# Kernel optimization log

Measured on AMD Instinct MI355X. Metric: run time of the kernel, lower is better.

## Reference

```python
import jax, jax.numpy as jnp
import numpy as np

NEG = -1e30  # log-zero surrogate (avoid -inf for stable grads)


def ctc_neg_log_like(log_probs, targets, input_lengths, target_lengths):
    """Standard CTC (blank=0) negative log-likelihood, mean over batch.
    Math-equivalent to k2 topo-compile + intersect_dense + log-semiring tot_scores.
    log_probs: [B,T,C] logits or log-probs (re-normalized, as GradExpNormalize does).
    """
    lp = jax.nn.log_softmax(log_probs, axis=-1)
    B, T, C = lp.shape
    S = targets.shape[1]
    L = 2 * S + 1  # blank-interleaved extended label sequence length
    ext = jnp.zeros((B, L), jnp.int32).at[:, 1::2].set(targets.astype(jnp.int32))
    prev2 = jnp.pad(ext[:, :-2], ((0, 0), (2, 0)), constant_values=-1)
    can_skip = (ext != prev2) & (ext != 0)  # skip transition allowed

    lp_tb = jnp.moveaxis(lp, 1, 0)  # [T,B,C] for scan over time
    start = jnp.full((B, L), NEG, lp.dtype).at[:, 0].set(0.0).at[:, 1].set(0.0)
    alpha0 = start + jnp.take_along_axis(lp_tb[0], ext, axis=1)  # [B,L]

    def step(alpha, xs):
        lp_t, t = xs
        emit_t = jnp.take_along_axis(lp_t, ext, axis=1)  # [B,L]
        s1 = jnp.pad(alpha[:, :-1], ((0, 0), (1, 0)), constant_values=NEG)
        s2 = jnp.where(can_skip,
                       jnp.pad(alpha[:, :-2], ((0, 0), (2, 0)), constant_values=NEG),
                       NEG)
        new = jnp.logaddexp(jnp.logaddexp(alpha, s1), s2) + emit_t
        # freeze alpha once past this utterance's length
        new = jnp.where((t < input_lengths)[:, None], new, alpha)
        return new, None

    ts = jnp.arange(1, T, dtype=jnp.int32)
    alpha, _ = jax.lax.scan(step, alpha0, (lp_tb[1:], ts))

    idx1 = (2 * target_lengths).astype(jnp.int32)
    idx2 = jnp.maximum(2 * target_lengths - 1, 0).astype(jnp.int32)
    a1 = jnp.take_along_axis(alpha, idx1[:, None], axis=1)[:, 0]
    a2 = jnp.take_along_axis(alpha, idx2[:, None], axis=1)[:, 0]
    a2 = jnp.where(target_lengths > 0, a2, NEG)
    tot_scores = jnp.logaddexp(a1, a2)  # per-utterance log-likelihood
    return -jnp.mean(tot_scores)  # reduction='mean'


def setup_inputs() -> dict:
    key = jax.random.key(0)
    k1, k2, k3, k4 = jax.random.split(key, 4)
    B, T, C, S = 64, 2048, 1024, 256
    log_probs = jax.random.normal(k1, (B, T, C), dtype=jnp.float32)
    targets = 1 + jax.random.randint(k2, (B, S), 0, C - 1, dtype=jnp.int32)  # labels in [1, C)
    input_lengths = jax.random.randint(k3, (B,), T // 2, T + 1, dtype=jnp.int32)
    target_lengths = jax.random.randint(k4, (B,), S // 2, S + 1, dtype=jnp.int32)
    return {"log_probs": log_probs, "targets": targets,
            "input_lengths": input_lengths, "target_lengths": target_lengths}


def reference(log_probs, targets, input_lengths, target_lengths):
    return ctc_neg_log_like(log_probs, targets, input_lengths, target_lengths)
```

## Files before the change

kernel.cpp:

```cpp
#include <hip/hip_runtime.h>
#include <math.h>

typedef __attribute__((ext_vector_type(4))) float f32x4;

#define SB() __builtin_amdgcn_sched_barrier(0)
#define WAITV(n)                                              \
  do {                                                        \
    asm volatile("s_waitcnt vmcnt(" #n ")" ::: "memory");     \
    SB();                                                     \
  } while (0)
#define LD4(dst, ptr, OFF)                                           \
  asm volatile("global_load_dwordx4 %0, %1, off offset:" OFF         \
               : "=v"(dst) : "v"(ptr) : "memory")
#define LD1(dst, ptr, OFF)                                           \
  asm volatile("global_load_dword %0, %1, off offset:" OFF           \
               : "=v"(dst) : "v"(ptr) : "memory")

__device__ inline float wave_max64(float v) {
#pragma unroll
  for (int off = 32; off > 0; off >>= 1) v = fmaxf(v, __shfl_xor(v, off, 64));
  return v;
}
__device__ inline float wave_sum64(float v) {
#pragma unroll
  for (int off = 32; off > 0; off >>= 1) v += __shfl_xor(v, off, 64);
  return v;
}
__device__ inline float wave_max_dpp(float x) {
  int xi = __float_as_int(x);
  x = fmaxf(x, __int_as_float(__builtin_amdgcn_update_dpp(xi, xi, 0x111, 0xf, 0xf, false)));
  xi = __float_as_int(x);
  x = fmaxf(x, __int_as_float(__builtin_amdgcn_update_dpp(xi, xi, 0x112, 0xf, 0xf, false)));
  xi = __float_as_int(x);
  x = fmaxf(x, __int_as_float(__builtin_amdgcn_update_dpp(xi, xi, 0x114, 0xf, 0xf, false)));
  xi = __float_as_int(x);
  x = fmaxf(x, __int_as_float(__builtin_amdgcn_update_dpp(xi, xi, 0x118, 0xf, 0xf, false)));
  xi = __float_as_int(x);
  x = fmaxf(x, __int_as_float(__builtin_amdgcn_update_dpp(xi, xi, 0x142, 0xa, 0xf, false)));
  xi = __float_as_int(x);
  x = fmaxf(x, __int_as_float(__builtin_amdgcn_update_dpp(xi, xi, 0x143, 0xc, 0xf, false)));
  return __int_as_float(__builtin_amdgcn_readlane(__float_as_int(x), 63));
}
__device__ inline float lane_shr1(float x) {
  return __int_as_float(__builtin_amdgcn_update_dpp(
      0, __float_as_int(x), 0x138, 0xf, 0xf, true));
}

__device__ __forceinline__ void k1_body(
    const float* __restrict__ lp, const int* __restrict__ targets,
    float* __restrict__ gw, int t0, int T, int Tc, int CB, int S,
    int b, int tq, float* rowbuf) {
  const int lane = threadIdx.x & 63;
  const int w = threadIdx.x >> 6;
  const int tloc = tq * 4 + w;
  const int t = t0 + tloc;
  if (t >= T) return;
  const int4 tg4 = *(const int4*)(targets + (size_t)b * S + 4 * lane);

  const float* row = lp + ((size_t)b * T + t) * 1024;
  const float4 v0 = *(const float4*)(row + 4 * lane);
  const float4 v1 = *(const float4*)(row + 256 + 4 * lane);
  const float4 v2 = *(const float4*)(row + 512 + 4 * lane);
  const float4 v3 = *(const float4*)(row + 768 + 4 * lane);
  float mx = fmaxf(fmaxf(fmaxf(v0.x, v0.y), fmaxf(v0.z, v0.w)),
                   fmaxf(fmaxf(v1.x, v1.y), fmaxf(v1.z, v1.w)));
  mx = fmaxf(mx, fmaxf(fmaxf(fmaxf(v2.x, v2.y), fmaxf(v2.z, v2.w)),
                       fmaxf(fmaxf(v3.x, v3.y), fmaxf(v3.z, v3.w))));
  mx = wave_max64(mx);
  float sm = __expf(v0.x - mx) + __expf(v0.y - mx) + __expf(v0.z - mx) +
             __expf(v0.w - mx) + __expf(v1.x - mx) + __expf(v1.y - mx) +
             __expf(v1.z - mx) + __expf(v1.w - mx) + __expf(v2.x - mx) +
             __expf(v2.y - mx) + __expf(v2.z - mx) + __expf(v2.w - mx) +
             __expf(v3.x - mx) + __expf(v3.y - mx) + __expf(v3.z - mx) +
             __expf(v3.w - mx);
  sm = wave_sum64(sm);
  const float lse = mx + __logf(sm);
  *(float4*)(rowbuf + 4 * lane) = v0;
  *(float4*)(rowbuf + 256 + 4 * lane) = v1;
  *(float4*)(rowbuf + 512 + 4 * lane) = v2;
  *(float4*)(rowbuf + 768 + 4 * lane) = v3;
  const float e0 = __expf(rowbuf[tg4.x] - lse);
  const float e1 = __expf(rowbuf[tg4.y] - lse);
  const float e2 = __expf(rowbuf[tg4.z] - lse);
  const float e3 = __expf(rowbuf[tg4.w] - lse);
  float* gr = gw + ((size_t)b * CB + tloc) * 272;
  *(float4*)(gr + 4 * lane) = make_float4(e0, e1, e2, e3);
  if (lane == 0) gr[256] = __expf(rowbuf[0] - lse);
}

__global__ __launch_bounds__(256) void k1_std(
    const float* __restrict__ lp, const int* __restrict__ targets,
    float* __restrict__ gw, int t0, int T, int Tc, int CB, int S) {
  __shared__ __align__(16) float rowbuf4[4][1024];
  k1_body(lp, targets, gw, t0, T, Tc, CB, S, blockIdx.y, blockIdx.x,
          rowbuf4[threadIdx.x >> 6]);
}

#define DECL8(P)                                                     \
  f32x4 P##v0, P##v1, P##v2, P##v3, P##v4, P##v5, P##v6, P##v7;      \
  float P##q0, P##q1, P##q2, P##q3, P##q4, P##q5, P##q6, P##q7;

#define ISS8(P)                                                      \
  do {                                                               \
    LD4(P##v0, gpA_, "0");    LD1(P##q0, gqA_, "0");                 \
    LD4(P##v1, gpA_, "1088"); LD1(P##q1, gqA_, "1088");              \
    LD4(P##v2, gpA_, "2176"); LD1(P##q2, gqA_, "2176");              \
    LD4(P##v3, gpA_, "3264"); LD1(P##q3, gqA_, "3264");              \
    LD4(P##v4, gpB_, "0");    LD1(P##q4, gqB_, "0");                 \
    LD4(P##v5, gpB_, "1088"); LD1(P##q5, gqB_, "1088");              \
    LD4(P##v6, gpB_, "2176"); LD1(P##q6, gqB_, "2176");              \
    LD4(P##v7, gpB_, "3264"); LD1(P##q7, gqB_, "3264");              \
    gpA_ += 2176; gqA_ += 2176; gpB_ += 2176; gqB_ += 2176;          \
  } while (0)

#define KSR(pv, qv)                                              \
  {                                                              \
    const float hm1 = lane_shr1(a7);                             \
    const float n0 = (a0 + hm1) * (qv);                          \
    const float n1 = __fmaf_rn(sk1, hm1, a1 + a0) * (pv).x;      \
    const float n2 = (a2 + a1) * (qv);                           \
    const float n3 = __fmaf_rn(sk3, a1, a3 + a2) * (pv).y;       \
    const float n4 = (a4 + a3) * (qv);                           \
    const float n5 = __fmaf_rn(sk5, a3, a5 + a4) * (pv).z;       \
    const float n6 = (a6 + a5) * (qv);                           \
    const float n7 = __fmaf_rn(sk7, a5, a7 + a6) * (pv).w;       \
    const float n8 = (a8 + a7) * (qv);                           \
    a0 = n0; a1 = n1; a2 = n2; a3 = n3; a4 = n4;                 \
    a5 = n5; a6 = n6; a7 = n7; a8 = n8;                          \
  }

#define RESC()                                                            \
  {                                                                       \
    float m_ = fmaxf(fmaxf(fmaxf(fmaxf(a0, a1), fmaxf(a2, a3)),           \
                           fmaxf(fmaxf(a4, a5), fmaxf(a6, a7))), a8);     \
    m_ = wave_max_dpp(m_);                                                \
    const int e_ =                                                        \
        (m_ > 0.f) ? (int)((__float_as_uint(m_) >> 23) & 255u) - 127 : 0; \
    a0 = ldexpf(a0, -e_); a1 = ldexpf(a1, -e_); a2 = ldexpf(a2, -e_);     \
    a3 = ldexpf(a3, -e_); a4 = ldexpf(a4, -e_); a5 = ldexpf(a5, -e_);     \
    a6 = ldexpf(a6, -e_); a7 = ldexpf(a7, -e_); a8 = ldexpf(a8, -e_);     \
    E += e_;                                                              \
  }

#define COMP8(P, rem)                                            \
  do {                                                           \
    if ((rem) >= 8) {                                            \
      KSR(P##v0, P##q0) KSR(P##v1, P##q1) KSR(P##v2, P##q2)      \
      KSR(P##v3, P##q3) KSR(P##v4, P##q4) KSR(P##v5, P##q5)      \
      KSR(P##v6, P##q6) KSR(P##v7, P##q7) RESC()                 \
    } else {                                                     \
      KSR(P##v0, P##q0)                                          \
      if ((rem) > 1) KSR(P##v1, P##q1)                           \
      if ((rem) > 2) KSR(P##v2, P##q2)                           \
      if ((rem) > 3) KSR(P##v3, P##q3)                           \
      if ((rem) > 4) KSR(P##v4, P##q4)                           \
      if ((rem) > 5) KSR(P##v5, P##q5)                           \
      if ((rem) > 6) KSR(P##v6, P##q6)                           \
      RESC()                                                     \
    }                                                            \
  } while (0)

template <int R0, int LAST>
__device__ __forceinline__ void k2_body(
    const float* __restrict__ gb, const int* __restrict__ targets,
    const int* __restrict__ in_len, const int* __restrict__ tgt_len,
    float* __restrict__ alpha_g, int* __restrict__ exp_g,
    float* __restrict__ tot, int b, int t0, int Tc, int S) {
  const int lane = threadIdx.x & 63;
  const int len = in_len[b];
  const int tl = tgt_len[b];
  const int* tg = targets + (size_t)b * S;
  const int4 mytg = *(const int4*)(tg + 4 * lane);
  const int tgm1 = (lane > 0) ? tg[4 * lane - 1] : -1;
  const float sk1 = (lane > 0 && mytg.x != tgm1) ? 1.f : 0.f;
  const float sk3 = (mytg.y != mytg.x) ? 1.f : 0.f;
  const float sk5 = (mytg.z != mytg.y) ? 1.f : 0.f;
  const float sk7 = (mytg.w != mytg.z) ? 1.f : 0.f;

  float a0 = 0.f, a1 = 0.f, a2 = 0.f, a3 = 0.f, a4 = 0.f, a5 = 0.f, a6 = 0.f,
        a7 = 0.f, a8 = 0.f;
  int E = 0;
  if (R0) {
    if (lane == 0) { a0 = gb[256]; a1 = gb[0]; }
  } else {
    const float* ap = alpha_g + (size_t)b * 520 + 8 * lane;
    a0 = ap[0]; a1 = ap[1]; a2 = ap[2]; a3 = ap[3];
    a4 = ap[4]; a5 = ap[5]; a6 = ap[6]; a7 = ap[7];
    a8 = (lane == 63) ? alpha_g[(size_t)b * 520 + 512] : 0.f;
    E = exp_g[b];
  }

  const int t_hi = min(t0 + Tc, len);
  int N = t_hi - (t0 + R0);
  if (N < 0) N = 0;
  const int G = (N + 7) >> 3;

  const float* gpA_ = gb + (size_t)R0 * 272 + 4 * lane;
  const float* gqA_ = gb + (size_t)R0 * 272 + 256;
  const float* gpB_ = gpA_ + 1088;
  const float* gqB_ = gqA_ + 1088;

  DECL8(A) DECL8(B)

  __builtin_amdgcn_s_setprio(1);
  asm volatile("s_waitcnt vmcnt(0) lgkmcnt(0)" ::: "memory");
  SB();
  ISS8(A); ISS8(B);

  for (int g = 0; g < G; g += 2) {
    WAITV(16);
    COMP8(A, N - 8 * g);
    ISS8(A);
    if (g + 1 < G) {
      WAITV(16);
      COMP8(B, N - 8 * (g + 1));
      ISS8(B);
    }
  }
  WAITV(0);
  __builtin_amdgcn_s_setprio(0);

  if constexpr (LAST) {
    __shared__ float fin[520];
    fin[8 * lane + 0] = a0; fin[8 * lane + 1] = a1;
    fin[8 * lane + 2] = a2; fin[8 * lane + 3] = a3;
    fin[8 * lane + 4] = a4; fin[8 * lane + 5] = a5;
    fin[8 * lane + 6] = a6; fin[8 * lane + 7] = a7;
    if (lane == 63) fin[512] = a8;
    asm volatile("s_waitcnt lgkmcnt(0)" ::: "memory");
    SB();
    if (lane == 0) {
      const int i1 = 2 * tl;
      const int i2 = (2 * tl - 1 > 0) ? (2 * tl - 1) : 0;
      float v = fin[i1] + ((tl > 0) ? fin[i2] : 0.f);
      v = fmaxf(v, 1e-37f);
      tot[b] = logf(v) + (float)E * 0.6931471805599453f;
    }
  } else {
    float* ap = alpha_g + (size_t)b * 520 + 8 * lane;
    ap[0] = a0; ap[1] = a1; ap[2] = a2; ap[3] = a3;
    ap[4] = a4; ap[5] = a5; ap[6] = a6; ap[7] = a7;
    if (lane == 63) alpha_g[(size_t)b * 520 + 512] = a8;
    if (lane == 0) exp_g[b] = E;
  }
}

template <int R0, int LAST>
__global__ __launch_bounds__(64, 1) void k2_std(
    const float* __restrict__ gbuf, const int* __restrict__ targets,
    const int* __restrict__ in_len, const int* __restrict__ tgt_len,
    float* __restrict__ alpha_g, int* __restrict__ exp_g,
    float* __restrict__ tot, int t0, int Tc, int CB, int S) {
  k2_body<R0, LAST>(gbuf + (size_t)blockIdx.x * CB * 272, targets, in_len,
                    tgt_len, alpha_g, exp_g, tot, blockIdx.x, t0, Tc, S);
}

template <int R0>
__global__ __launch_bounds__(256, 1) void fused_k(
    const float* __restrict__ lp, const int* __restrict__ targets,
    const int* __restrict__ in_len, const int* __restrict__ tgt_len,
    float* __restrict__ alpha_g, int* __restrict__ exp_g,
    float* __restrict__ tot, const float* __restrict__ gprev,
    float* __restrict__ gcur, int t0k2, int t0k1, int T, int Tc, int CB,
    int S, int TQ4) {
  __shared__ __align__(16) float rowbuf4[4][1024];
  if (blockIdx.x < 64) {
    if (threadIdx.x >= 64) return;
    k2_body<R0, 0>(gprev + (size_t)blockIdx.x * CB * 272, targets, in_len,
                   tgt_len, alpha_g, exp_g, tot, blockIdx.x, t0k2, Tc, S);
    return;
  }
  const int id = blockIdx.x - 64;
  const int b = id / TQ4;
  const int tq = id - b * TQ4;
  k1_body(lp, targets, gcur, t0k1, T, Tc, CB, S, b, tq,
          rowbuf4[threadIdx.x >> 6]);
}

__global__ void k3_mean(const float* __restrict__ tot, float* __restrict__ out,
                        int B) {
  float v = (threadIdx.x < B) ? tot[threadIdx.x] : 0.0f;
  v = wave_sum64(v);
  if (threadIdx.x == 0) out[0] = -v / (float)B;
}

extern "C" void kernel_launch(void* const* d_in, const int* in_sizes, int n_in,
                              void* d_out, int out_size, void* d_ws,
                              size_t ws_size, hipStream_t stream) {
  const float* lp = (const float*)d_in[0];
  const int* targets = (const int*)d_in[1];
  const int* in_len = (const int*)d_in[2];
  const int* tgt_len = (const int*)d_in[3];
  float* out = (float*)d_out;

  const int B = in_sizes[2];
  const int S = in_sizes[1] / B;
  const int C = 1024;
  const int T = (int)((size_t)in_sizes[0] / ((size_t)B * C));

  const size_t headf = 64 + 64 + (size_t)64 * 520;
  int Tc = 512;
  if (Tc > T) Tc = T;
  while (Tc > 64) {
    const size_t need =
        headf * 4 + 2 * (size_t)64 * (Tc + 64) * 272 * 4;
    if (need <= ws_size) break;
    Tc >>= 1;
  }
  const int CB = Tc + 64;
  const int nch = (T + Tc - 1) / Tc;
  const int TQ4 = Tc / 4;

  float* tot = (float*)d_ws;
  int* exp_g = (int*)(tot + 64);
  float* alpha_g = (float*)(exp_g + 64);
  float* g0 = alpha_g + (size_t)64 * 520;
  const size_t BUF = (size_t)64 * CB * 272;
  float* gbuf[2] = {g0, g0 + BUF};

  if (nch == 1) {
    k1_std<<<dim3(TQ4, B), 256, 0, stream>>>(lp, targets, gbuf[0], 0, T, Tc,
                                             CB, S);
    k2_std<1, 1><<<B, 64, 0, stream>>>(gbuf[0], targets, in_len, tgt_len,
                                       alpha_g, exp_g, tot, 0, Tc, CB, S);
  } else {
    k1_std<<<dim3(TQ4, B), 256, 0, stream>>>(lp, targets, gbuf[0], 0, T, Tc,
                                             CB, S);
    for (int c = 1; c < nch; ++c) {
      const int t0k2 = (c - 1) * Tc;
      const int t0k1 = c * Tc;
      const dim3 grid(64 + TQ4 * B);
      if (c == 1)
        fused_k<1><<<grid, 256, 0, stream>>>(
            lp, targets, in_len, tgt_len, alpha_g, exp_g, tot,
            gbuf[(c - 1) & 1], gbuf[c & 1], t0k2, t0k1, T, Tc, CB, S, TQ4);
      else
        fused_k<0><<<grid, 256, 0, stream>>>(
            lp, targets, in_len, tgt_len, alpha_g, exp_g, tot,
            gbuf[(c - 1) & 1], gbuf[c & 1], t0k2, t0k1, T, Tc, CB, S, TQ4);
    }
    const int cl = nch - 1;
    k2_std<0, 1><<<B, 64, 0, stream>>>(gbuf[cl & 1], targets, in_len, tgt_len,
                                       alpha_g, exp_g, tot, cl * Tc, Tc, CB,
                                       S);
  }
  k3_mean<<<1, 64, 0, stream>>>(tot, out, B);
}
```

Measured before the change: 233.5 us.

## Pack eight waves per block and triple-buffer the alpha recursion loads

Blocks now hold 8 waves (512 threads) instead of 4. The recursion stage (k2) packs 8 batch rows per block, so it runs on 8 blocks instead of 64 single-wave blocks. The k2 inner loop moves from double to triple buffering of the 8-step load groups (vmcnt 32), which keeps more loads in flight to hide global latency on the serial alpha chain. The risks are higher register pressure from the third buffer set, and 8 recursion waves now sharing one CU instead of spreading across 64 CUs, which could slow the latency-bound sequential part.

```diff
diff --git a/kernel.cpp b/kernel.cpp
--- a/kernel.cpp
+++ b/kernel.cpp
@@ -46,13 +46,13 @@
       0, __float_as_int(x), 0x138, 0xf, 0xf, true));
 }
 
-__device__ __forceinline__ void k1_body(
+__device__ __forceinline__ void k1_body8(
     const float* __restrict__ lp, const int* __restrict__ targets,
-    float* __restrict__ gw, int t0, int T, int Tc, int CB, int S,
+    float* __restrict__ gw, int t0, int T, int CB, int S,
     int b, int tq, float* rowbuf) {
   const int lane = threadIdx.x & 63;
   const int w = threadIdx.x >> 6;
-  const int tloc = tq * 4 + w;
+  const int tloc = tq * 8 + w;
   const int t = t0 + tloc;
   if (t >= T) return;
   const int4 tg4 = *(const int4*)(targets + (size_t)b * S + 4 * lane);
@@ -88,12 +88,12 @@
   if (lane == 0) gr[256] = __expf(rowbuf[0] - lse);
 }
 
-__global__ __launch_bounds__(256) void k1_std(
+__global__ __launch_bounds__(512, 2) void k1_std8(
     const float* __restrict__ lp, const int* __restrict__ targets,
-    float* __restrict__ gw, int t0, int T, int Tc, int CB, int S) {
-  __shared__ __align__(16) float rowbuf4[4][1024];
-  k1_body(lp, targets, gw, t0, T, Tc, CB, S, blockIdx.y, blockIdx.x,
-          rowbuf4[threadIdx.x >> 6]);
+    float* __restrict__ gw, int t0, int T, int CB, int S) {
+  __shared__ __align__(16) float lds[8192];
+  k1_body8(lp, targets, gw, t0, T, CB, S, blockIdx.y, blockIdx.x,
+           lds + (threadIdx.x >> 6) * 1024);
 }
 
 #define DECL8(P)                                                     \
@@ -165,7 +165,7 @@
     const float* __restrict__ gb, const int* __restrict__ targets,
     const int* __restrict__ in_len, const int* __restrict__ tgt_len,
     float* __restrict__ alpha_g, int* __restrict__ exp_g,
-    float* __restrict__ tot, int b, int t0, int Tc, int S) {
+    float* __restrict__ tot, int b, int t0, int Tc, int S, float* fin) {
   const int lane = threadIdx.x & 63;
   const int len = in_len[b];
   const int tl = tgt_len[b];
@@ -200,28 +200,32 @@
   const float* gpB_ = gpA_ + 1088;
   const float* gqB_ = gqA_ + 1088;
 
-  DECL8(A) DECL8(B)
+  DECL8(A) DECL8(B) DECL8(C)
 
   __builtin_amdgcn_s_setprio(1);
   asm volatile("s_waitcnt vmcnt(0) lgkmcnt(0)" ::: "memory");
   SB();
-  ISS8(A); ISS8(B);
-
-  for (int g = 0; g < G; g += 2) {
-    WAITV(16);
+  ISS8(A); ISS8(B); ISS8(C);
+
+  for (int g = 0; g < G; g += 3) {
+    WAITV(32);
     COMP8(A, N - 8 * g);
     ISS8(A);
     if (g + 1 < G) {
-      WAITV(16);
+      WAITV(32);
       COMP8(B, N - 8 * (g + 1));
       ISS8(B);
     }
+    if (g + 2 < G) {
+      WAITV(32);
+      COMP8(C, N - 8 * (g + 2));
+      ISS8(C);
+    }
   }
   WAITV(0);
   __builtin_amdgcn_s_setprio(0);
 
   if constexpr (LAST) {
-    __shared__ float fin[520];
     fin[8 * lane + 0] = a0; fin[8 * lane + 1] = a1;
     fin[8 * lane + 2] = a2; fin[8 * lane + 3] = a3;
     fin[8 * lane + 4] = a4; fin[8 * lane + 5] = a5;
@@ -246,35 +250,38 @@
 }
 
 template <int R0, int LAST>
-__global__ __launch_bounds__(64, 1) void k2_std(
+__global__ __launch_bounds__(512, 2) void k2_std8(
     const float* __restrict__ gbuf, const int* __restrict__ targets,
     const int* __restrict__ in_len, const int* __restrict__ tgt_len,
     float* __restrict__ alpha_g, int* __restrict__ exp_g,
     float* __restrict__ tot, int t0, int Tc, int CB, int S) {
-  k2_body<R0, LAST>(gbuf + (size_t)blockIdx.x * CB * 272, targets, in_len,
-                    tgt_len, alpha_g, exp_g, tot, blockIdx.x, t0, Tc, S);
+  __shared__ float fin[4160];
+  const int w = threadIdx.x >> 6;
+  const int b = blockIdx.x * 8 + w;
+  k2_body<R0, LAST>(gbuf + (size_t)b * CB * 272, targets, in_len, tgt_len,
+                    alpha_g, exp_g, tot, b, t0, Tc, S, fin + w * 520);
 }
 
 template <int R0>
-__global__ __launch_bounds__(256, 1) void fused_k(
+__global__ __launch_bounds__(512, 2) void fused8(
     const float* __restrict__ lp, const int* __restrict__ targets,
     const int* __restrict__ in_len, const int* __restrict__ tgt_len,
     float* __restrict__ alpha_g, int* __restrict__ exp_g,
     float* __restrict__ tot, const float* __restrict__ gprev,
     float* __restrict__ gcur, int t0k2, int t0k1, int T, int Tc, int CB,
-    int S, int TQ4) {
-  __shared__ __align__(16) float rowbuf4[4][1024];
-  if (blockIdx.x < 64) {
-    if (threadIdx.x >= 64) return;
-    k2_body<R0, 0>(gprev + (size_t)blockIdx.x * CB * 272, targets, in_len,
-                   tgt_len, alpha_g, exp_g, tot, blockIdx.x, t0k2, Tc, S);
+    int S, int TQ8) {
+  __shared__ __align__(16) float lds[8192];
+  const int w = threadIdx.x >> 6;
+  if (blockIdx.x < 8) {
+    const int b = blockIdx.x * 8 + w;
+    k2_body<R0, 0>(gprev + (size_t)b * CB * 272, targets, in_len, tgt_len,
+                   alpha_g, exp_g, tot, b, t0k2, Tc, S, lds + w * 520);
     return;
   }
-  const int id = blockIdx.x - 64;
-  const int b = id / TQ4;
-  const int tq = id - b * TQ4;
-  k1_body(lp, targets, gcur, t0k1, T, Tc, CB, S, b, tq,
-          rowbuf4[threadIdx.x >> 6]);
+  const int id = blockIdx.x - 8;
+  const int b = id / TQ8;
+  const int tq = id - b * TQ8;
+  k1_body8(lp, targets, gcur, t0k1, T, CB, S, b, tq, lds + w * 1024);
 }
 
 __global__ void k3_mean(const float* __restrict__ tot, float* __restrict__ out,
@@ -302,14 +309,13 @@
   int Tc = 512;
   if (Tc > T) Tc = T;
   while (Tc > 64) {
-    const size_t need =
-        headf * 4 + 2 * (size_t)64 * (Tc + 64) * 272 * 4;
+    const size_t need = headf * 4 + 2 * (size_t)64 * (Tc + 64) * 272 * 4;
     if (need <= ws_size) break;
     Tc >>= 1;
   }
   const int CB = Tc + 64;
   const int nch = (T + Tc - 1) / Tc;
-  const int TQ4 = Tc / 4;
+  const int TQ8 = Tc / 8;
 
   float* tot = (float*)d_ws;
   int* exp_g = (int*)(tot + 64);
@@ -319,30 +325,30 @@
   float* gbuf[2] = {g0, g0 + BUF};
 
   if (nch == 1) {
-    k1_std<<<dim3(TQ4, B), 256, 0, stream>>>(lp, targets, gbuf[0], 0, T, Tc,
-                                             CB, S);
-    k2_std<1, 1><<<B, 64, 0, stream>>>(gbuf[0], targets, in_len, tgt_len,
-                                       alpha_g, exp_g, tot, 0, Tc, CB, S);
+    k1_std8<<<dim3(TQ8, B), 512, 0, stream>>>(lp, targets, gbuf[0], 0, T, CB,
+                                              S);
+    k2_std8<1, 1><<<8, 512, 0, stream>>>(gbuf[0], targets, in_len, tgt_len,
+                                         alpha_g, exp_g, tot, 0, Tc, CB, S);
   } else {
-    k1_std<<<dim3(TQ4, B), 256, 0, stream>>>(lp, targets, gbuf[0], 0, T, Tc,
-                                             CB, S);
+    k1_std8<<<dim3(TQ8, B), 512, 0, stream>>>(lp, targets, gbuf[0], 0, T, CB,
+                                              S);
     for (int c = 1; c < nch; ++c) {
       const int t0k2 = (c - 1) * Tc;
       const int t0k1 = c * Tc;
-      const dim3 grid(64 + TQ4 * B);
+      const dim3 grid(8 + TQ8 * B);
       if (c == 1)
-        fused_k<1><<<grid, 256, 0, stream>>>(
+        fused8<1><<<grid, 512, 0, stream>>>(
             lp, targets, in_len, tgt_len, alpha_g, exp_g, tot,
-            gbuf[(c - 1) & 1], gbuf[c & 1], t0k2, t0k1, T, Tc, CB, S, TQ4);
+            gbuf[(c - 1) & 1], gbuf[c & 1], t0k2, t0k1, T, Tc, CB, S, TQ8);
       else
-        fused_k<0><<<grid, 256, 0, stream>>>(
+        fused8<0><<<grid, 512, 0, stream>>>(
             lp, targets, in_len, tgt_len, alpha_g, exp_g, tot,
-            gbuf[(c - 1) & 1], gbuf[c & 1], t0k2, t0k1, T, Tc, CB, S, TQ4);
+            gbuf[(c - 1) & 1], gbuf[c & 1], t0k2, t0k1, T, Tc, CB, S, TQ8);
     }
     const int cl = nch - 1;
-    k2_std<0, 1><<<B, 64, 0, stream>>>(gbuf[cl & 1], targets, in_len, tgt_len,
-                                       alpha_g, exp_g, tot, cl * Tc, Tc, CB,
-                                       S);
+    k2_std8<0, 1><<<8, 512, 0, stream>>>(gbuf[cl & 1], targets, in_len,
+                                         tgt_len, alpha_g, exp_g, tot,
+                                         cl * Tc, Tc, CB, S);
   }
   k3_mean<<<1, 64, 0, stream>>>(tot, out, B);
 }
```

New measurement: 324.4 us. 38.9% more time.

## Pair two utterances per recursion wave and split blank emissions into separate array

Applied to the files above, without the earlier changes.

The serial CTC forward recursion now runs two batch items interleaved in one wave, so 32 recursion waves replace 64 and each wave has two independent dependency chains to hide latency. The blank emission probabilities move out of the padded 272-float rows into a contiguous per-batch array, which allows vector loads for blanks and 256-float label rows. The cost is twice the register state per wave, a deeper load pipeline, and a loop length set by the longer of the two utterances.

```diff
diff --git a/kernel.cpp b/kernel.cpp
--- a/kernel.cpp
+++ b/kernel.cpp
@@ -11,9 +11,6 @@
   } while (0)
 #define LD4(dst, ptr, OFF)                                           \
   asm volatile("global_load_dwordx4 %0, %1, off offset:" OFF         \
-               : "=v"(dst) : "v"(ptr) : "memory")
-#define LD1(dst, ptr, OFF)                                           \
-  asm volatile("global_load_dword %0, %1, off offset:" OFF           \
                : "=v"(dst) : "v"(ptr) : "memory")
 
 __device__ inline float wave_max64(float v) {
@@ -48,8 +45,8 @@
 
 __device__ __forceinline__ void k1_body(
     const float* __restrict__ lp, const int* __restrict__ targets,
-    float* __restrict__ gw, int t0, int T, int Tc, int CB, int S,
-    int b, int tq, float* rowbuf) {
+    float* __restrict__ gw, float* __restrict__ qw, int t0, int T, int CB,
+    int QS, int S, int b, int tq, float* rowbuf) {
   const int lane = threadIdx.x & 63;
   const int w = threadIdx.x >> 6;
   const int tloc = tq * 4 + w;
@@ -83,198 +80,256 @@
   const float e1 = __expf(rowbuf[tg4.y] - lse);
   const float e2 = __expf(rowbuf[tg4.z] - lse);
   const float e3 = __expf(rowbuf[tg4.w] - lse);
-  float* gr = gw + ((size_t)b * CB + tloc) * 272;
+  float* gr = gw + ((size_t)b * CB + tloc) * 256;
   *(float4*)(gr + 4 * lane) = make_float4(e0, e1, e2, e3);
-  if (lane == 0) gr[256] = __expf(rowbuf[0] - lse);
+  if (lane == 0) qw[(size_t)b * QS + tloc] = __expf(rowbuf[0] - lse);
 }
 
 __global__ __launch_bounds__(256) void k1_std(
     const float* __restrict__ lp, const int* __restrict__ targets,
-    float* __restrict__ gw, int t0, int T, int Tc, int CB, int S) {
+    float* __restrict__ gw, float* __restrict__ qw, int t0, int T, int CB,
+    int QS, int S) {
   __shared__ __align__(16) float rowbuf4[4][1024];
-  k1_body(lp, targets, gw, t0, T, Tc, CB, S, blockIdx.y, blockIdx.x,
+  k1_body(lp, targets, gw, qw, t0, T, CB, QS, S, blockIdx.y, blockIdx.x,
           rowbuf4[threadIdx.x >> 6]);
 }
 
-#define DECL8(P)                                                     \
-  f32x4 P##v0, P##v1, P##v2, P##v3, P##v4, P##v5, P##v6, P##v7;      \
-  float P##q0, P##q1, P##q2, P##q3, P##q4, P##q5, P##q6, P##q7;
-
-#define ISS8(P)                                                      \
+#define DECLSET(P) \
+  f32x4 P##v0, P##v1, P##v2, P##v3, P##v4, P##v5, P##v6, P##v7, P##qL, P##qH;
+
+#define ISS8(P, B)                                                   \
   do {                                                               \
-    LD4(P##v0, gpA_, "0");    LD1(P##q0, gqA_, "0");                 \
-    LD4(P##v1, gpA_, "1088"); LD1(P##q1, gqA_, "1088");              \
-    LD4(P##v2, gpA_, "2176"); LD1(P##q2, gqA_, "2176");              \
-    LD4(P##v3, gpA_, "3264"); LD1(P##q3, gqA_, "3264");              \
-    LD4(P##v4, gpB_, "0");    LD1(P##q4, gqB_, "0");                 \
-    LD4(P##v5, gpB_, "1088"); LD1(P##q5, gqB_, "1088");              \
-    LD4(P##v6, gpB_, "2176"); LD1(P##q6, gqB_, "2176");              \
-    LD4(P##v7, gpB_, "3264"); LD1(P##q7, gqB_, "3264");              \
-    gpA_ += 2176; gqA_ += 2176; gpB_ += 2176; gqB_ += 2176;          \
+    LD4(P##v0, B##gp0, "0");    LD4(P##v1, B##gp0, "1024");          \
+    LD4(P##v2, B##gp0, "2048"); LD4(P##v3, B##gp0, "3072");          \
+    LD4(P##v4, B##gp1, "0");    LD4(P##v5, B##gp1, "1024");          \
+    LD4(P##v6, B##gp1, "2048"); LD4(P##v7, B##gp1, "3072");          \
+    LD4(P##qL, B##gq, "0");     LD4(P##qH, B##gq, "16");             \
+    B##gp0 += 2048; B##gp1 += 2048; B##gq += 8;                      \
   } while (0)
 
-#define KSR(pv, qv)                                              \
-  {                                                              \
-    const float hm1 = lane_shr1(a7);                             \
-    const float n0 = (a0 + hm1) * (qv);                          \
-    const float n1 = __fmaf_rn(sk1, hm1, a1 + a0) * (pv).x;      \
-    const float n2 = (a2 + a1) * (qv);                           \
-    const float n3 = __fmaf_rn(sk3, a1, a3 + a2) * (pv).y;       \
-    const float n4 = (a4 + a3) * (qv);                           \
-    const float n5 = __fmaf_rn(sk5, a3, a5 + a4) * (pv).z;       \
-    const float n6 = (a6 + a5) * (qv);                           \
-    const float n7 = __fmaf_rn(sk7, a5, a7 + a6) * (pv).w;       \
-    const float n8 = (a8 + a7) * (qv);                           \
-    a0 = n0; a1 = n1; a2 = n2; a3 = n3; a4 = n4;                 \
-    a5 = n5; a6 = n6; a7 = n7; a8 = n8;                          \
-  }
-
-#define RESC()                                                            \
-  {                                                                       \
-    float m_ = fmaxf(fmaxf(fmaxf(fmaxf(a0, a1), fmaxf(a2, a3)),           \
-                           fmaxf(fmaxf(a4, a5), fmaxf(a6, a7))), a8);     \
-    m_ = wave_max_dpp(m_);                                                \
-    const int e_ =                                                        \
-        (m_ > 0.f) ? (int)((__float_as_uint(m_) >> 23) & 255u) - 127 : 0; \
-    a0 = ldexpf(a0, -e_); a1 = ldexpf(a1, -e_); a2 = ldexpf(a2, -e_);     \
-    a3 = ldexpf(a3, -e_); a4 = ldexpf(a4, -e_); a5 = ldexpf(a5, -e_);     \
-    a6 = ldexpf(a6, -e_); a7 = ldexpf(a7, -e_); a8 = ldexpf(a8, -e_);     \
-    E += e_;                                                              \
-  }
-
-#define COMP8(P, rem)                                            \
-  do {                                                           \
-    if ((rem) >= 8) {                                            \
-      KSR(P##v0, P##q0) KSR(P##v1, P##q1) KSR(P##v2, P##q2)      \
-      KSR(P##v3, P##q3) KSR(P##v4, P##q4) KSR(P##v5, P##q5)      \
-      KSR(P##v6, P##q6) KSR(P##v7, P##q7) RESC()                 \
-    } else {                                                     \
-      KSR(P##v0, P##q0)                                          \
-      if ((rem) > 1) KSR(P##v1, P##q1)                           \
-      if ((rem) > 2) KSR(P##v2, P##q2)                           \
-      if ((rem) > 3) KSR(P##v3, P##q3)                           \
-      if ((rem) > 4) KSR(P##v4, P##q4)                           \
-      if ((rem) > 5) KSR(P##v5, P##q5)                           \
-      if ((rem) > 6) KSR(P##v6, P##q6)                           \
-      RESC()                                                     \
-    }                                                            \
+#define KSR(B, pv, qv)                                                 \
+  {                                                                    \
+    const float hm1 = lane_shr1(B##a7);                                \
+    const float n0 = (B##a0 + hm1) * (qv);                             \
+    const float n1 = __fmaf_rn(B##sk1, hm1, B##a1 + B##a0) * (pv).x;   \
+    const float n2 = (B##a2 + B##a1) * (qv);                           \
+    const float n3 = __fmaf_rn(B##sk3, B##a1, B##a3 + B##a2) * (pv).y; \
+    const float n4 = (B##a4 + B##a3) * (qv);                           \
+    const float n5 = __fmaf_rn(B##sk5, B##a3, B##a5 + B##a4) * (pv).z; \
+    const float n6 = (B##a6 + B##a5) * (qv);                           \
+    const float n7 = __fmaf_rn(B##sk7, B##a5, B##a7 + B##a6) * (pv).w; \
+    const float n8 = (B##a8 + B##a7) * (qv);                           \
+    B##a0 = n0; B##a1 = n1; B##a2 = n2; B##a3 = n3; B##a4 = n4;        \
+    B##a5 = n5; B##a6 = n6; B##a7 = n7; B##a8 = n8;                    \
+  }
+
+#define RESC(B)                                                              \
+  {                                                                          \
+    float m_ = fmaxf(fmaxf(fmaxf(fmaxf(B##a0, B##a1), fmaxf(B##a2, B##a3)),  \
+                           fmaxf(fmaxf(B##a4, B##a5), fmaxf(B##a6, B##a7))), \
+                     B##a8);                                                 \
+    m_ = wave_max_dpp(m_);                                                   \
+    const int e_ =                                                           \
+        (m_ > 0.f) ? (int)((__float_as_uint(m_) >> 23) & 255u) - 127 : 0;    \
+    B##a0 = ldexpf(B##a0, -e_); B##a1 = ldexpf(B##a1, -e_);                  \
+    B##a2 = ldexpf(B##a2, -e_); B##a3 = ldexpf(B##a3, -e_);                  \
+    B##a4 = ldexpf(B##a4, -e_); B##a5 = ldexpf(B##a5, -e_);                  \
+    B##a6 = ldexpf(B##a6, -e_); B##a7 = ldexpf(B##a7, -e_);                  \
+    B##a8 = ldexpf(B##a8, -e_);                                              \
+    B##E += e_;                                                              \
+  }
+
+#define COMP8(P, B, rem)                                             \
+  do {                                                               \
+    if ((rem) > 0) {                                                 \
+      if ((rem) >= 8) {                                              \
+        KSR(B, P##v0, (P##qL).x) KSR(B, P##v1, (P##qL).y)            \
+        KSR(B, P##v2, (P##qL).z) KSR(B, P##v3, (P##qL).w)            \
+        KSR(B, P##v4, (P##qH).x) KSR(B, P##v5, (P##qH).y)            \
+        KSR(B, P##v6, (P##qH).z) KSR(B, P##v7, (P##qH).w)            \
+        RESC(B)                                                      \
+      } else {                                                       \
+        KSR(B, P##v0, (P##qL).x)                                     \
+        if ((rem) > 1) KSR(B, P##v1, (P##qL).y)                      \
+        if ((rem) > 2) KSR(B, P##v2, (P##qL).z)                      \
+        if ((rem) > 3) KSR(B, P##v3, (P##qL).w)                      \
+        if ((rem) > 4) KSR(B, P##v4, (P##qH).x)                      \
+        if ((rem) > 5) KSR(B, P##v5, (P##qH).y)                      \
+        if ((rem) > 6) KSR(B, P##v6, (P##qH).z)                      \
+        RESC(B)                                                      \
+      }                                                              \
+    }                                                                \
   } while (0)
 
+#define SAVEB(B, bidx)                                                      \
+  {                                                                         \
+    float* ap = alpha_g + (size_t)(bidx)*520 + 8 * lane;                    \
+    ap[0] = B##a0; ap[1] = B##a1; ap[2] = B##a2; ap[3] = B##a3;             \
+    ap[4] = B##a4; ap[5] = B##a5; ap[6] = B##a6; ap[7] = B##a7;             \
+    if (lane == 63) alpha_g[(size_t)(bidx)*520 + 512] = B##a8;              \
+    if (lane == 0) exp_g[bidx] = B##E;                                      \
+  }
+
 template <int R0, int LAST>
-__device__ __forceinline__ void k2_body(
-    const float* __restrict__ gb, const int* __restrict__ targets,
-    const int* __restrict__ in_len, const int* __restrict__ tgt_len,
-    float* __restrict__ alpha_g, int* __restrict__ exp_g,
-    float* __restrict__ tot, int b, int t0, int Tc, int S) {
+__device__ __forceinline__ void k2_pair_body(
+    const float* __restrict__ gwc, const float* __restrict__ qwc,
+    const int* __restrict__ targets, const int* __restrict__ in_len,
+    const int* __restrict__ tgt_len, float* __restrict__ alpha_g,
+    int* __restrict__ exp_g, float* __restrict__ tot, int bA, int t0, int Tc,
+    int CB, int QS, int S, float* finA, float* finB) {
   const int lane = threadIdx.x & 63;
-  const int len = in_len[b];
-  const int tl = tgt_len[b];
-  const int* tg = targets + (size_t)b * S;
-  const int4 mytg = *(const int4*)(tg + 4 * lane);
-  const int tgm1 = (lane > 0) ? tg[4 * lane - 1] : -1;
-  const float sk1 = (lane > 0 && mytg.x != tgm1) ? 1.f : 0.f;
-  const float sk3 = (mytg.y != mytg.x) ? 1.f : 0.f;
-  const float sk5 = (mytg.z != mytg.y) ? 1.f : 0.f;
-  const float sk7 = (mytg.w != mytg.z) ? 1.f : 0.f;
-
-  float a0 = 0.f, a1 = 0.f, a2 = 0.f, a3 = 0.f, a4 = 0.f, a5 = 0.f, a6 = 0.f,
-        a7 = 0.f, a8 = 0.f;
-  int E = 0;
+  const int bB = bA + 1;
+  const float* gA_ = gwc + (size_t)bA * CB * 256;
+  const float* gB_ = gwc + (size_t)bB * CB * 256;
+  const float* qA_ = qwc + (size_t)bA * QS;
+  const float* qB_ = qwc + (size_t)bB * QS;
+
+  float Ask1, Ask3, Ask5, Ask7, Bsk1, Bsk3, Bsk5, Bsk7;
+  {
+    const int* tg_ = targets + (size_t)bA * S;
+    const int4 t4_ = *(const int4*)(tg_ + 4 * lane);
+    const int tm1_ = (lane > 0) ? tg_[4 * lane - 1] : -1;
+    Ask1 = (lane > 0 && t4_.x != tm1_) ? 1.f : 0.f;
+    Ask3 = (t4_.y != t4_.x) ? 1.f : 0.f;
+    Ask5 = (t4_.z != t4_.y) ? 1.f : 0.f;
+    Ask7 = (t4_.w != t4_.z) ? 1.f : 0.f;
+  }
+  {
+    const int* tg_ = targets + (size_t)bB * S;
+    const int4 t4_ = *(const int4*)(tg_ + 4 * lane);
+    const int tm1_ = (lane > 0) ? tg_[4 * lane - 1] : -1;
+    Bsk1 = (lane > 0 && t4_.x != tm1_) ? 1.f : 0.f;
+    Bsk3 = (t4_.y != t4_.x) ? 1.f : 0.f;
+    Bsk5 = (t4_.z != t4_.y) ? 1.f : 0.f;
+    Bsk7 = (t4_.w != t4_.z) ? 1.f : 0.f;
+  }
+
+  float Aa0 = 0.f, Aa1 = 0.f, Aa2 = 0.f, Aa3 = 0.f, Aa4 = 0.f, Aa5 = 0.f,
+        Aa6 = 0.f, Aa7 = 0.f, Aa8 = 0.f;
+  float Ba0 = 0.f, Ba1 = 0.f, Ba2 = 0.f, Ba3 = 0.f, Ba4 = 0.f, Ba5 = 0.f,
+        Ba6 = 0.f, Ba7 = 0.f, Ba8 = 0.f;
+  int AE = 0, BE = 0;
   if (R0) {
-    if (lane == 0) { a0 = gb[256]; a1 = gb[0]; }
+    if (lane == 0) {
+      Aa0 = qA_[0]; Aa1 = gA_[0];
+      Ba0 = qB_[0]; Ba1 = gB_[0];
+    }
   } else {
-    const float* ap = alpha_g + (size_t)b * 520 + 8 * lane;
-    a0 = ap[0]; a1 = ap[1]; a2 = ap[2]; a3 = ap[3];
-    a4 = ap[4]; a5 = ap[5]; a6 = ap[6]; a7 = ap[7];
-    a8 = (lane == 63) ? alpha_g[(size_t)b * 520 + 512] : 0.f;
-    E = exp_g[b];
-  }
-
-  const int t_hi = min(t0 + Tc, len);
-  int N = t_hi - (t0 + R0);
-  if (N < 0) N = 0;
-  const int G = (N + 7) >> 3;
-
-  const float* gpA_ = gb + (size_t)R0 * 272 + 4 * lane;
-  const float* gqA_ = gb + (size_t)R0 * 272 + 256;
-  const float* gpB_ = gpA_ + 1088;
-  const float* gqB_ = gqA_ + 1088;
-
-  DECL8(A) DECL8(B)
+    const float* ap = alpha_g + (size_t)bA * 520 + 8 * lane;
+    Aa0 = ap[0]; Aa1 = ap[1]; Aa2 = ap[2]; Aa3 = ap[3];
+    Aa4 = ap[4]; Aa5 = ap[5]; Aa6 = ap[6]; Aa7 = ap[7];
+    const float* bp = alpha_g + (size_t)bB * 520 + 8 * lane;
+    Ba0 = bp[0]; Ba1 = bp[1]; Ba2 = bp[2]; Ba3 = bp[3];
+    Ba4 = bp[4]; Ba5 = bp[5]; Ba6 = bp[6]; Ba7 = bp[7];
+    if (lane == 63) {
+      Aa8 = alpha_g[(size_t)bA * 520 + 512];
+      Ba8 = alpha_g[(size_t)bB * 520 + 512];
+    }
+    AE = exp_g[bA]; BE = exp_g[bB];
+  }
+
+  const int lenA = in_len[bA], lenB = in_len[bB];
+  const int tlA = tgt_len[bA], tlB = tgt_len[bB];
+  int NA = min(t0 + Tc, lenA) - (t0 + R0); if (NA < 0) NA = 0;
+  int NB = min(t0 + Tc, lenB) - (t0 + R0); if (NB < 0) NB = 0;
+  const int G = ((NA > NB ? NA : NB) + 7) >> 3;
+
+  const float* Agp0 = gA_ + (size_t)R0 * 256 + 4 * lane;
+  const float* Agp1 = Agp0 + 1024;
+  const float* Agq = qA_ + R0;
+  const float* Bgp0 = gB_ + (size_t)R0 * 256 + 4 * lane;
+  const float* Bgp1 = Bgp0 + 1024;
+  const float* Bgq = qB_ + R0;
+
+  DECLSET(XA) DECLSET(XB) DECLSET(YA) DECLSET(YB)
 
   __builtin_amdgcn_s_setprio(1);
   asm volatile("s_waitcnt vmcnt(0) lgkmcnt(0)" ::: "memory");
   SB();
-  ISS8(A); ISS8(B);
+  ISS8(XA, A); ISS8(XB, B); ISS8(YA, A); ISS8(YB, B);
 
   for (int g = 0; g < G; g += 2) {
-    WAITV(16);
-    COMP8(A, N - 8 * g);
-    ISS8(A);
-    if (g + 1 < G) {
-      WAITV(16);
-      COMP8(B, N - 8 * (g + 1));
-      ISS8(B);
-    }
+    WAITV(20);
+    COMP8(XA, A, NA - 8 * g);
+    COMP8(XB, B, NB - 8 * g);
+    ISS8(XA, A); ISS8(XB, B);
+    WAITV(20);
+    COMP8(YA, A, NA - 8 * (g + 1));
+    COMP8(YB, B, NB - 8 * (g + 1));
+    ISS8(YA, A); ISS8(YB, B);
   }
   WAITV(0);
   __builtin_amdgcn_s_setprio(0);
 
   if constexpr (LAST) {
-    __shared__ float fin[520];
-    fin[8 * lane + 0] = a0; fin[8 * lane + 1] = a1;
-    fin[8 * lane + 2] = a2; fin[8 * lane + 3] = a3;
-    fin[8 * lane + 4] = a4; fin[8 * lane + 5] = a5;
-    fin[8 * lane + 6] = a6; fin[8 * lane + 7] = a7;
-    if (lane == 63) fin[512] = a8;
+    finA[8 * lane + 0] = Aa0; finA[8 * lane + 1] = Aa1;
+    finA[8 * lane + 2] = Aa2; finA[8 * lane + 3] = Aa3;
+    finA[8 * lane + 4] = Aa4; finA[8 * lane + 5] = Aa5;
+    finA[8 * lane + 6] = Aa6; finA[8 * lane + 7] = Aa7;
+    finB[8 * lane + 0] = Ba0; finB[8 * lane + 1] = Ba1;
+    finB[8 * lane + 2] = Ba2; finB[8 * lane + 3] = Ba3;
+    finB[8 * lane + 4] = Ba4; finB[8 * lane + 5] = Ba5;
+    finB[8 * lane + 6] = Ba6; finB[8 * lane + 7] = Ba7;
+    if (lane == 63) { finA[512] = Aa8; finB[512] = Ba8; }
     asm volatile("s_waitcnt lgkmcnt(0)" ::: "memory");
     SB();
     if (lane == 0) {
-      const int i1 = 2 * tl;
-      const int i2 = (2 * tl - 1 > 0) ? (2 * tl - 1) : 0;
-      float v = fin[i1] + ((tl > 0) ? fin[i2] : 0.f);
-      v = fmaxf(v, 1e-37f);
-      tot[b] = logf(v) + (float)E * 0.6931471805599453f;
+      {
+        const int i1 = 2 * tlA;
+        const int i2 = (2 * tlA - 1 > 0) ? (2 * tlA - 1) : 0;
+        float v = finA[i1] + ((tlA > 0) ? finA[i2] : 0.f);
+        v = fmaxf(v, 1e-37f);
+        tot[bA] = logf(v) + (float)AE * 0.6931471805599453f;
+      }
+      {
+        const int i1 = 2 * tlB;
+        const int i2 = (2 * tlB - 1 > 0) ? (2 * tlB - 1) : 0;
+        float v = finB[i1] + ((tlB > 0) ? finB[i2] : 0.f);
+        v = fmaxf(v, 1e-37f);
+        tot[bB] = logf(v) + (float)BE * 0.6931471805599453f;
+      }
     }
   } else {
-    float* ap = alpha_g + (size_t)b * 520 + 8 * lane;
-    ap[0] = a0; ap[1] = a1; ap[2] = a2; ap[3] = a3;
-    ap[4] = a4; ap[5] = a5; ap[6] = a6; ap[7] = a7;
-    if (lane == 63) alpha_g[(size_t)b * 520 + 512] = a8;
-    if (lane == 0) exp_g[b] = E;
+    SAVEB(A, bA)
+    SAVEB(B, bB)
   }
 }
 
 template <int R0, int LAST>
-__global__ __launch_bounds__(64, 1) void k2_std(
-    const float* __restrict__ gbuf, const int* __restrict__ targets,
-    const int* __restrict__ in_len, const int* __restrict__ tgt_len,
-    float* __restrict__ alpha_g, int* __restrict__ exp_g,
-    float* __restrict__ tot, int t0, int Tc, int CB, int S) {
-  k2_body<R0, LAST>(gbuf + (size_t)blockIdx.x * CB * 272, targets, in_len,
-                    tgt_len, alpha_g, exp_g, tot, blockIdx.x, t0, Tc, S);
+__global__ __launch_bounds__(64, 1) void k2p_std(
+    const float* __restrict__ gwc, const float* __restrict__ qwc,
+    const int* __restrict__ targets, const int* __restrict__ in_len,
+    const int* __restrict__ tgt_len, float* __restrict__ alpha_g,
+    int* __restrict__ exp_g, float* __restrict__ tot, int t0, int Tc, int CB,
+    int QS, int S) {
+  __shared__ float fin[1040];
+  k2_pair_body<R0, LAST>(gwc, qwc, targets, in_len, tgt_len, alpha_g, exp_g,
+                         tot, blockIdx.x * 2, t0, Tc, CB, QS, S, fin,
+                         fin + 520);
 }
 
 template <int R0>
-__global__ __launch_bounds__(256, 1) void fused_k(
+__global__ __launch_bounds__(256, 1) void fusedp(
     const float* __restrict__ lp, const int* __restrict__ targets,
     const int* __restrict__ in_len, const int* __restrict__ tgt_len,
     float* __restrict__ alpha_g, int* __restrict__ exp_g,
     float* __restrict__ tot, const float* __restrict__ gprev,
-    float* __restrict__ gcur, int t0k2, int t0k1, int T, int Tc, int CB,
-    int S, int TQ4) {
-  __shared__ __align__(16) float rowbuf4[4][1024];
-  if (blockIdx.x < 64) {
+    const float* __restrict__ qprev, float* __restrict__ gcur,
+    float* __restrict__ qcur, int t0k2, int t0k1, int T, int Tc, int CB,
+    int QS, int S, int TQ4) {
+  __shared__ __align__(16) float lds[4096];
+  if (blockIdx.x < 32) {
     if (threadIdx.x >= 64) return;
-    k2_body<R0, 0>(gprev + (size_t)blockIdx.x * CB * 272, targets, in_len,
-                   tgt_len, alpha_g, exp_g, tot, blockIdx.x, t0k2, Tc, S);
+    k2_pair_body<R0, 0>(gprev, qprev, targets, in_len, tgt_len, alpha_g,
+                        exp_g, tot, blockIdx.x * 2, t0k2, Tc, CB, QS, S,
+                        nullptr, nullptr);
     return;
   }
-  const int id = blockIdx.x - 64;
+  const int id = blockIdx.x - 32;
   const int b = id / TQ4;
   const int tq = id - b * TQ4;
-  k1_body(lp, targets, gcur, t0k1, T, Tc, CB, S, b, tq,
-          rowbuf4[threadIdx.x >> 6]);
+  k1_body(lp, targets, gcur, qcur, t0k1, T, CB, QS, S, b, tq,
+          lds + (threadIdx.x >> 6) * 1024);
 }
 
 __global__ void k3_mean(const float* __restrict__ tot, float* __restrict__ out,
@@ -301,48 +356,56 @@
   const size_t headf = 64 + 64 + (size_t)64 * 520;
   int Tc = 512;
   if (Tc > T) Tc = T;
-  while (Tc > 64) {
-    const size_t need =
-        headf * 4 + 2 * (size_t)64 * (Tc + 64) * 272 * 4;
-    if (need <= ws_size) break;
+  int CB = 0, QS = 0;
+  while (Tc >= 64) {
+    CB = Tc + 64;
+    QS = Tc + 64;
+    const size_t need = (headf + 2 * (size_t)64 * QS) * 4 +
+                        2 * (size_t)64 * CB * 1024 + (size_t)80 * 1024;
+    if (need <= ws_size || Tc == 64) break;
     Tc >>= 1;
   }
-  const int CB = Tc + 64;
   const int nch = (T + Tc - 1) / Tc;
   const int TQ4 = Tc / 4;
 
   float* tot = (float*)d_ws;
   int* exp_g = (int*)(tot + 64);
   float* alpha_g = (float*)(exp_g + 64);
-  float* g0 = alpha_g + (size_t)64 * 520;
-  const size_t BUF = (size_t)64 * CB * 272;
-  float* gbuf[2] = {g0, g0 + BUF};
+  float* q0 = alpha_g + (size_t)64 * 520;
+  float* q1 = q0 + (size_t)64 * QS;
+  float* g0 = q1 + (size_t)64 * QS;
+  float* g1 = g0 + (size_t)64 * CB * 256;
+  float* gbuf[2] = {g0, g1};
+  float* qbuf[2] = {q0, q1};
 
   if (nch == 1) {
-    k1_std<<<dim3(TQ4, B), 256, 0, stream>>>(lp, targets, gbuf[0], 0, T, Tc,
-                                             CB, S);
-    k2_std<1, 1><<<B, 64, 0, stream>>>(gbuf[0], targets, in_len, tgt_len,
-                                       alpha_g, exp_g, tot, 0, Tc, CB, S);
+    k1_std<<<dim3(TQ4, B), 256, 0, stream>>>(lp, targets, gbuf[0], qbuf[0], 0,
+                                             T, CB, QS, S);
+    k2p_std<1, 1><<<32, 64, 0, stream>>>(gbuf[0], qbuf[0], targets, in_len,
+                                         tgt_len, alpha_g, exp_g, tot, 0, Tc,
+                                         CB, QS, S);
   } else {
-    k1_std<<<dim3(TQ4, B), 256, 0, stream>>>(lp, targets, gbuf[0], 0, T, Tc,
-                                             CB, S);
+    k1_std<<<dim3(TQ4, B), 256, 0, stream>>>(lp, targets, gbuf[0], qbuf[0], 0,
+                                             T, CB, QS, S);
     for (int c = 1; c < nch; ++c) {
       const int t0k2 = (c - 1) * Tc;
       const int t0k1 = c * Tc;
-      const dim3 grid(64 + TQ4 * B);
+      const dim3 grid(32 + TQ4 * B);
       if (c == 1)
-        fused_k<1><<<grid, 256, 0, stream>>>(
+        fusedp<1><<<grid, 256, 0, stream>>>(
             lp, targets, in_len, tgt_len, alpha_g, exp_g, tot,
-            gbuf[(c - 1) & 1], gbuf[c & 1], t0k2, t0k1, T, Tc, CB, S, TQ4);
+            gbuf[(c - 1) & 1], qbuf[(c - 1) & 1], gbuf[c & 1], qbuf[c & 1],
+            t0k2, t0k1, T, Tc, CB, QS, S, TQ4);
       else
-        fused_k<0><<<grid, 256, 0, stream>>>(
+        fusedp<0><<<grid, 256, 0, stream>>>(
             lp, targets, in_len, tgt_len, alpha_g, exp_g, tot,
-            gbuf[(c - 1) & 1], gbuf[c & 1], t0k2, t0k1, T, Tc, CB, S, TQ4);
+            gbuf[(c - 1) & 1], qbuf[(c - 1) & 1], gbuf[c & 1], qbuf[c & 1],
+            t0k2, t0k1, T, Tc, CB, QS, S, TQ4);
     }
     const int cl = nch - 1;
-    k2_std<0, 1><<<B, 64, 0, stream>>>(gbuf[cl & 1], targets, in_len, tgt_len,
-                                       alpha_g, exp_g, tot, cl * Tc, Tc, CB,
-                                       S);
+    k2p_std<0, 1><<<32, 64, 0, stream>>>(gbuf[cl & 1], qbuf[cl & 1], targets,
+                                         in_len, tgt_len, alpha_g, exp_g, tot,
+                                         cl * Tc, Tc, CB, QS, S);
   }
   k3_mean<<<1, 64, 0, stream>>>(tot, out, B);
 }
```

Measured after the change: 386.9 us. +65.7%, slower.
